# Optimization experiments

Hardware: AMD Instinct MI355X
Metric: run time of the kernel (lower is better)

Reference implementation:

```python
import jax, jax.numpy as jnp
import numpy as np

N_NODES = 100000
N_EDGES = 1600000
D_IN = 128
D_HID = 128
D_OUT = 128
N_LAYERS = 4


def setup_inputs() -> dict:
    key = jax.random.key(0)
    ks = jax.random.split(key, 8)
    x = jax.random.normal(ks[0], (N_NODES, D_IN), dtype=jnp.float32)
    edge_index = jax.random.randint(ks[1], (2, N_EDGES), 0, N_NODES, dtype=jnp.int64)
    s = 1.0 / np.sqrt(D_IN)
    # All layers are 128->128, so stack weights: [L, in, out]
    W_lin = jax.random.uniform(ks[2], (N_LAYERS, D_IN, D_HID), minval=-s, maxval=s, dtype=jnp.float32)
    W_film = jax.random.uniform(ks[3], (N_LAYERS, D_IN, 2 * D_HID), minval=-s, maxval=s, dtype=jnp.float32)
    b_film = jax.random.uniform(ks[4], (N_LAYERS, 2 * D_HID), minval=-s, maxval=s, dtype=jnp.float32)
    W_skip = jax.random.uniform(ks[5], (N_LAYERS, D_IN, D_HID), minval=-s, maxval=s, dtype=jnp.float32)
    W_fskip = jax.random.uniform(ks[6], (N_LAYERS, D_IN, 2 * D_HID), minval=-s, maxval=s, dtype=jnp.float32)
    return {"x": x, "edge_index": edge_index, "W_lin": W_lin, "W_film": W_film,
            "b_film": b_film, "W_skip": W_skip, "W_fskip": W_fskip}


def _film_conv(x, src, dst, deg_inv, W_l, W_f, b_f, W_s, W_fs, c):
    # skip path: FiLM-modulated self transform
    bg_s = x @ W_fs                       # [N, 2C], no bias
    beta_s, gamma_s = bg_s[:, :c], bg_s[:, c:]
    out = jax.nn.relu(gamma_s * (x @ W_s) + beta_s)
    # message path: FiLM params from target node, features from source node
    bg = x @ W_f + b_f                    # [N, 2C]
    beta, gamma = bg[:, :c], bg[:, c:]
    h = x @ W_l                           # [N, C]
    msg = jax.nn.relu(gamma[dst] * h[src] + beta[dst])  # [E, C]
    agg = jax.ops.segment_sum(msg, dst, num_segments=x.shape[0]) * deg_inv  # mean aggr
    return out + agg


def reference(x, edge_index, W_lin, W_film, b_film, W_skip, W_fskip):
    src, dst = edge_index[0], edge_index[1]
    n = x.shape[0]
    deg = jax.ops.segment_sum(jnp.ones((src.shape[0],), x.dtype), dst, num_segments=n)
    deg_inv = (1.0 / jnp.maximum(deg, 1.0))[:, None]   # clamp(min=1) like PyG mean
    for l in range(N_LAYERS):
        x = _film_conv(x, src, dst, deg_inv, W_lin[l], W_film[l], b_film[l],
                       W_skip[l], W_fskip[l], D_HID)
        if l < N_LAYERS - 1:
            x = jax.nn.relu(x)
    return x
```

## Files before the change

### kernel.cpp

```cpp
#include <hip/hip_runtime.h>
#include <hip/hip_bf16.h>

#define N_NODES 100000
#define N_PAD   100096
#define N_EDGES 1600000
#define NXCD    8
#define NRANGE  ((N_NODES + NXCD - 1) / NXCD)
#define NSLICE  256
#define MTILES  (N_PAD / 128)
#define MTQ     ((MTILES + 7) / 8)
#define GEMM_GRID (8 * 7 * MTQ)

typedef __bf16 bf16x8 __attribute__((ext_vector_type(8)));
typedef float  f32x4  __attribute__((ext_vector_type(4)));

__device__ __forceinline__ void gload16(const void* g, void* s) {
    __builtin_amdgcn_global_load_lds(
        (const __attribute__((address_space(1))) unsigned int*)g,
        (__attribute__((address_space(3))) unsigned int*)s, 16, 0, 0);
}

__device__ __forceinline__ float2 bf2f(unsigned p) {
    float2 r;
    union { unsigned u; float f; } a, b;
    a.u = p << 16;
    b.u = p & 0xffff0000u;
    r.x = a.f; r.y = b.f;
    return r;
}
__device__ __forceinline__ unsigned f2bf2(float x, float y) {
    unsigned lo = (unsigned)__builtin_bit_cast(unsigned short, __float2bfloat16(x));
    unsigned hi = (unsigned)__builtin_bit_cast(unsigned short, __float2bfloat16(y));
    return lo | (hi << 16);
}

__global__ void detect_kernel(const unsigned* __restrict__ e, int* __restrict__ flag) {
    __shared__ int nz;
    if (threadIdx.x == 0) nz = 0;
    __syncthreads();
    int local = 0;
    for (int i = threadIdx.x; i < 1024; i += blockDim.x)
        if (e[2 * i + 1] != 0) local = 1;
    if (local) atomicOr(&nz, 1);
    __syncthreads();
    if (threadIdx.x == 0) *flag = (nz == 0) ? 1 : 0;
}

__device__ __forceinline__ int edge_at(const unsigned* __restrict__ e, long idx, int is64) {
    return (int)(is64 ? e[2 * idx] : e[idx]);
}

__global__ void hist_kernel(const unsigned* __restrict__ e, const int* __restrict__ flag,
                            int* __restrict__ counts) {
    int i = blockIdx.x * blockDim.x + threadIdx.x;
    if (i >= N_EDGES) return;
    int is64 = *flag;
    int d = edge_at(e, (long)N_EDGES + i, is64);
    atomicAdd(&counts[d], 1);
}

__global__ void scan1_kernel(const int* __restrict__ counts, int* __restrict__ blockSums) {
    __shared__ int red[256];
    int base = blockIdx.x * 1024;
    int sum = 0;
    for (int i = threadIdx.x; i < 1024; i += 256) {
        int idx = base + i;
        sum += (idx < N_NODES) ? counts[idx] : 0;
    }
    red[threadIdx.x] = sum;
    __syncthreads();
    for (int s = 128; s > 0; s >>= 1) {
        if (threadIdx.x < s) red[threadIdx.x] += red[threadIdx.x + s];
        __syncthreads();
    }
    if (threadIdx.x == 0) blockSums[blockIdx.x] = red[0];
}

__global__ void scan2_kernel(int* __restrict__ blockSums, int nb, int* __restrict__ row_ptr) {
    int run = 0;
    for (int i = 0; i < nb; ++i) { int v = blockSums[i]; blockSums[i] = run; run += v; }
    row_ptr[N_NODES] = run;
}

__global__ void scan3_kernel(const int* __restrict__ counts, const int* __restrict__ blockSums,
                             int* __restrict__ row_ptr, int* __restrict__ cursor,
                             float* __restrict__ deg_inv) {
    __shared__ int lds[256];
    int base = blockIdx.x * 1024;
    int t = threadIdx.x;
    int v[4];
    int s = 0;
    for (int i = 0; i < 4; ++i) {
        int idx = base + t * 4 + i;
        v[i] = (idx < N_NODES) ? counts[idx] : 0;
        s += v[i];
    }
    lds[t] = s;
    __syncthreads();
    for (int off = 1; off < 256; off <<= 1) {
        int add = (t >= off) ? lds[t - off] : 0;
        __syncthreads();
        lds[t] += add;
        __syncthreads();
    }
    int excl = lds[t] - s + blockSums[blockIdx.x];
    for (int i = 0; i < 4; ++i) {
        int idx = base + t * 4 + i;
        if (idx < N_NODES) {
            row_ptr[idx] = excl;
            cursor[idx]  = excl;
            deg_inv[idx] = 1.0f / fmaxf((float)v[i], 1.0f);
            excl += v[i];
        }
    }
}

__global__ __launch_bounds__(256) void fill2_kernel(
    const unsigned* __restrict__ e, const int* __restrict__ flag,
    int* __restrict__ cursor, int* __restrict__ csr_src) {
    const int r     = blockIdx.x & (NXCD - 1);
    const int slice = blockIdx.x >> 3;
    const int lo = r * NRANGE;
    const int hi = min(lo + NRANGE, N_NODES);
    const int is64 = *flag;
    const int per = (N_EDGES + NSLICE - 1) / NSLICE;
    const int i0 = slice * per;
    const int i1 = min(i0 + per, N_EDGES);
    for (int i = i0 + (int)threadIdx.x; i < i1; i += 256) {
        int d = edge_at(e, (long)N_EDGES + i, is64);
        if (d >= lo && d < hi) {
            int s = edge_at(e, (long)i, is64);
            int pos = atomicAdd(&cursor[d], 1);
            csr_src[pos] = s;
        }
    }
}

__global__ void bt_prep_kernel(const float* __restrict__ Wl, const float* __restrict__ Wf,
                               const float* __restrict__ Ws, const float* __restrict__ Wfs,
                               __hip_bfloat16* __restrict__ Bt) {
    int idx = blockIdx.x * 256 + threadIdx.x;
    if (idx >= 4 * 768 * 128) return;
    int k   = idx % 128;
    int row = (idx / 128) % 768;
    int lay = idx / (128 * 768);
    float w;
    if (row < 128) {
        w = Wl[(size_t)lay * 16384 + k * 128 + row];
    } else if (row < 384) {
        w = Wf[(size_t)lay * 32768 + k * 256 + (row - 128)];
    } else {
        int rr = row - 384;
        int g = rr >> 4, within = rr & 15;
        int kind = g % 3;
        int c = (g / 3) * 16 + within;
        if (kind == 0)      w = Ws [(size_t)lay * 16384 + k * 128 + c];
        else if (kind == 1) w = Wfs[(size_t)lay * 32768 + k * 256 + c];
        else                w = Wfs[(size_t)lay * 32768 + k * 256 + 128 + c];
    }
    Bt[idx] = __float2bfloat16(w);
}

__global__ void cast_kernel(const float* __restrict__ x, unsigned* __restrict__ A2) {
    long i = (long)blockIdx.x * 256 + threadIdx.x;
    if (i >= (long)N_NODES * 64) return;
    float2 v = ((const float2*)x)[i];
    A2[i] = f2bf2(v.x, v.y);
}

__global__ __launch_bounds__(256, 2) void fused_gemm_kernel(
    const __hip_bfloat16* __restrict__ A,
    const __hip_bfloat16* __restrict__ Bt,
    const float* __restrict__ bfilm,
    __hip_bfloat16* __restrict__ hbuf,
    __hip_bfloat16* __restrict__ bgbuf,
    __hip_bfloat16* __restrict__ skbh)
{
    __shared__ alignas(16) unsigned char lds_raw[32768];
    unsigned char* ldsA = lds_raw;
    unsigned char* ldsB = lds_raw + 16384;

    const int b   = blockIdx.x;
    const int r8  = b & 7;
    const int q   = b >> 3;
    const int jt  = q % 7;
    const int mt  = (q / 7) * 8 + r8;
    if (mt >= MTILES) return;

    const int t  = threadIdx.x;
    const long node0 = (long)mt * 128;
    const int w  = t >> 6, l = t & 63;
    const int wm = w >> 1, wn = w & 1;
    const int lr = l & 15;
    const int kq16 = (l >> 4) << 4;
    const int sw = (lr & 7) << 4;

    const int sr  = t >> 3;
    const int scb = (t & 7) << 4;
    const int scbs = scb ^ ((sr & 7) << 4);

    const char* Abase = (const char*)A;

    if (jt < 3) {
        const char* Bbase = (const char*)Bt + (size_t)(jt * 128) * 256;
        f32x4 acc[4][4];
        #pragma unroll
        for (int mi = 0; mi < 4; ++mi)
            #pragma unroll
            for (int ni = 0; ni < 4; ++ni)
                #pragma unroll
                for (int j = 0; j < 4; ++j) acc[mi][ni][j] = 0.f;

        #pragma unroll
        for (int ks = 0; ks < 2; ++ks) {
            const int k0 = ks * 64;
            #pragma unroll
            for (int i = 0; i < 4; ++i) {
                const int r = (i << 5) + sr;
                gload16(Abase + (node0 + r) * 256 + (size_t)k0 * 2 + scbs,
                        ldsA + (((i << 8) + t) << 4));
                gload16(Bbase + (size_t)r * 256 + (size_t)k0 * 2 + scbs,
                        ldsB + (((i << 8) + t) << 4));
            }
            __syncthreads();

            #pragma unroll
            for (int kh = 0; kh < 2; ++kh) {
                const int kbs = ((kh << 6) + kq16) ^ sw;
                bf16x8 af[4], bfr[4];
                #pragma unroll
                for (int mi = 0; mi < 4; ++mi)
                    af[mi] = *(const bf16x8*)(ldsA + (wm * 64 + mi * 16 + lr) * 128 + kbs);
                #pragma unroll
                for (int ni = 0; ni < 4; ++ni)
                    bfr[ni] = *(const bf16x8*)(ldsB + (wn * 64 + ni * 16 + lr) * 128 + kbs);
                #pragma unroll
                for (int mi = 0; mi < 4; ++mi)
                    #pragma unroll
                    for (int ni = 0; ni < 4; ++ni)
                        acc[mi][ni] = __builtin_amdgcn_mfma_f32_16x16x32_bf16(
                            af[mi], bfr[ni], acc[mi][ni], 0, 0, 0);
            }
            __syncthreads();
        }

        const int col = lr;
        const int rb  = (l >> 4) << 2;
        if (jt == 0) {
            #pragma unroll
            for (int mi = 0; mi < 4; ++mi)
                #pragma unroll
                for (int ni = 0; ni < 4; ++ni) {
                    const int n = wn * 64 + ni * 16 + col;
                    #pragma unroll
                    for (int j = 0; j < 4; ++j) {
                        long node = node0 + wm * 64 + mi * 16 + rb + j;
                        if (node < N_NODES)
                            hbuf[node * 128 + n] = __float2bfloat16(acc[mi][ni][j]);
                    }
                }
        } else {
            const int c0 = (jt - 1) * 128;
            #pragma unroll
            for (int mi = 0; mi < 4; ++mi)
                #pragma unroll
                for (int ni = 0; ni < 4; ++ni) {
                    const int n = wn * 64 + ni * 16 + col;
                    const float bb = bfilm[c0 + n];
                    #pragma unroll
                    for (int j = 0; j < 4; ++j) {
                        long node = node0 + wm * 64 + mi * 16 + rb + j;
                        if (node < N_NODES)
                            bgbuf[node * 256 + c0 + n] = __float2bfloat16(acc[mi][ni][j] + bb);
                    }
                }
        }
    } else {
        const int jt2 = jt - 3;
        const char* Bbase = (const char*)Bt + (size_t)(384 + jt2 * 96) * 256;
        f32x4 acc[4][3];
        #pragma unroll
        for (int mi = 0; mi < 4; ++mi)
            #pragma unroll
            for (int ni = 0; ni < 3; ++ni)
                #pragma unroll
                for (int j = 0; j < 4; ++j) acc[mi][ni][j] = 0.f;

        #pragma unroll
        for (int ks = 0; ks < 2; ++ks) {
            const int k0 = ks * 64;
            #pragma unroll
            for (int i = 0; i < 4; ++i) {
                const int r = (i << 5) + sr;
                gload16(Abase + (node0 + r) * 256 + (size_t)k0 * 2 + scbs,
                        ldsA + (((i << 8) + t) << 4));
            }
            #pragma unroll
            for (int i = 0; i < 3; ++i) {
                const int r = (i << 5) + sr;
                gload16(Bbase + (size_t)r * 256 + (size_t)k0 * 2 + scbs,
                        ldsB + (((i << 8) + t) << 4));
            }
            __syncthreads();

            #pragma unroll
            for (int kh = 0; kh < 2; ++kh) {
                const int kbs = ((kh << 6) + kq16) ^ sw;
                bf16x8 af[4], bfr[3];
                #pragma unroll
                for (int mi = 0; mi < 4; ++mi)
                    af[mi] = *(const bf16x8*)(ldsA + (wm * 64 + mi * 16 + lr) * 128 + kbs);
                #pragma unroll
                for (int ni = 0; ni < 3; ++ni)
                    bfr[ni] = *(const bf16x8*)(ldsB + (wn * 48 + ni * 16 + lr) * 128 + kbs);
                #pragma unroll
                for (int mi = 0; mi < 4; ++mi)
                    #pragma unroll
                    for (int ni = 0; ni < 3; ++ni)
                        acc[mi][ni] = __builtin_amdgcn_mfma_f32_16x16x32_bf16(
                            af[mi], bfr[ni], acc[mi][ni], 0, 0, 0);
            }
            __syncthreads();
        }

        const int c  = (2 * jt2 + wn) * 16 + lr;
        const int rb = (l >> 4) << 2;
        #pragma unroll
        for (int mi = 0; mi < 4; ++mi)
            #pragma unroll
            for (int j = 0; j < 4; ++j) {
                long node = node0 + wm * 64 + mi * 16 + rb + j;
                if (node < N_NODES) {
                    float o = fmaxf(acc[mi][2][j] * acc[mi][0][j] + acc[mi][1][j], 0.f);
                    skbh[node * 128 + c] = __float2bfloat16(o);
                }
            }
    }
}

__global__ __launch_bounds__(256) void agg_kernel(
    const uint2* __restrict__ h22,
    const uint2* __restrict__ bgu2,
    const int* __restrict__ row_ptr, const int* __restrict__ csr_src,
    const float* __restrict__ deg_inv,
    const uint2* __restrict__ sku2,
    uint2* __restrict__ An2,
    float4* __restrict__ fo4)
{
    const int t = threadIdx.x;
    const int v = blockIdx.x * 4 + (t >> 6);
    const int l = t & 63;
    const int half = l >> 5;
    const unsigned c = l & 31;

    const uint2 bu = bgu2[(size_t)v * 64 + c];
    const uint2 gu = bgu2[(size_t)v * 64 + 32 + c];
    const float2 be01 = bf2f(bu.x), be23 = bf2f(bu.y);
    const float2 ga01 = bf2f(gu.x), ga23 = bf2f(gu.y);
    const float dinv = deg_inv[v];

    const int b = row_ptr[v];
    const int e = row_ptr[v + 1];
    const int ne = e - b;
    const int npair = ne >> 1;

    f32x4 ac0 = {0,0,0,0}, ac1 = {0,0,0,0}, ac2 = {0,0,0,0}, ac3 = {0,0,0,0};

    const int* cp = csr_src + b + half;

#define ACC(A_, P_) do {                                   \
        float2 h01 = bf2f((P_).x), h23 = bf2f((P_).y);     \
        (A_)[0] += fmaxf(ga01.x * h01.x + be01.x, 0.f);    \
        (A_)[1] += fmaxf(ga01.y * h01.y + be01.y, 0.f);    \
        (A_)[2] += fmaxf(ga23.x * h23.x + be23.x, 0.f);    \
        (A_)[3] += fmaxf(ga23.y * h23.y + be23.y, 0.f);    \
    } while (0)

    int pi = 0;
    for (; pi + 8 <= npair; pi += 8) {
        unsigned s[8];
        uint2 p[8];
        #pragma unroll
        for (int u = 0; u < 8; ++u) s[u] = (unsigned)cp[2 * (pi + u)];
        #pragma unroll
        for (int u = 0; u < 8; ++u) p[u] = h22[s[u] * 32u + c];
        ACC(ac0, p[0]); ACC(ac1, p[1]); ACC(ac2, p[2]); ACC(ac3, p[3]);
        ACC(ac0, p[4]); ACC(ac1, p[5]); ACC(ac2, p[6]); ACC(ac3, p[7]);
    }
    for (; pi + 4 <= npair; pi += 4) {
        unsigned s[4];
        uint2 p[4];
        #pragma unroll
        for (int u = 0; u < 4; ++u) s[u] = (unsigned)cp[2 * (pi + u)];
        #pragma unroll
        for (int u = 0; u < 4; ++u) p[u] = h22[s[u] * 32u + c];
        ACC(ac0, p[0]); ACC(ac1, p[1]); ACC(ac2, p[2]); ACC(ac3, p[3]);
    }
    for (; pi < npair; ++pi) {
        const unsigned s0 = (unsigned)cp[2 * pi];
        const uint2 p0 = h22[s0 * 32u + c];
        ACC(ac0, p0);
    }
    if ((ne & 1) && half == 0) {
        const unsigned s0 = (unsigned)csr_src[e - 1];
        const uint2 p0 = h22[s0 * 32u + c];
        ACC(ac1, p0);
    }
#undef ACC

    float r0 = (ac0[0] + ac1[0]) + (ac2[0] + ac3[0]);
    float r1 = (ac0[1] + ac1[1]) + (ac2[1] + ac3[1]);
    float r2 = (ac0[2] + ac1[2]) + (ac2[2] + ac3[2]);
    float r3 = (ac0[3] + ac1[3]) + (ac2[3] + ac3[3]);
    r0 += __shfl_xor(r0, 32);
    r1 += __shfl_xor(r1, 32);
    r2 += __shfl_xor(r2, 32);
    r3 += __shfl_xor(r3, 32);

    const uint2 sk = sku2[(size_t)v * 32 + c];
    const float2 s01 = bf2f(sk.x), s23 = bf2f(sk.y);
    const float o0 = s01.x + r0 * dinv;
    const float o1 = s01.y + r1 * dinv;
    const float o2 = s23.x + r2 * dinv;
    const float o3 = s23.y + r3 * dinv;

    if (half == 0) {
        if (An2) {
            An2[(size_t)v * 32 + c] = make_uint2(f2bf2(o0, o1), f2bf2(o2, o3));
        } else {
            fo4[(size_t)v * 32 + c] = make_float4(o0, o1, o2, o3);
        }
    }
}

extern "C" void kernel_launch(void* const* d_in, const int* in_sizes, int n_in,
                              void* d_out, int out_size, void* d_ws, size_t ws_size,
                              hipStream_t stream) {
    const float*    x_in    = (const float*)d_in[0];
    const unsigned* eidx    = (const unsigned*)d_in[1];
    const float*    W_lin   = (const float*)d_in[2];
    const float*    W_film  = (const float*)d_in[3];
    const float*    b_film  = (const float*)d_in[4];
    const float*    W_skip  = (const float*)d_in[5];
    const float*    W_fskip = (const float*)d_in[6];
    float*          out     = (float*)d_out;

    char* ws = (char*)d_ws;
    size_t off = 0;
    auto alloc = [&](size_t bytes) -> void* {
        void* p = ws + off;
        off = (off + bytes + 255) & ~(size_t)255;
        return p;
    };
    int*   flag      = (int*)alloc(4);
    int*   counts    = (int*)alloc((size_t)N_NODES * 4);
    int*   row_ptr   = (int*)alloc((size_t)(N_NODES + 1) * 4);
    int*   cursor    = (int*)alloc((size_t)N_NODES * 4);
    int*   blockSums = (int*)alloc(128 * 4);
    float* deg_inv   = (float*)alloc((size_t)N_NODES * 4);
    int*   csr_src   = (int*)alloc((size_t)N_EDGES * 4);
    __hip_bfloat16* Abuf  = (__hip_bfloat16*)alloc((size_t)N_PAD * 128 * 2);
    __hip_bfloat16* BtAll = (__hip_bfloat16*)alloc((size_t)4 * 768 * 128 * 2);
    __hip_bfloat16* hbuf  = (__hip_bfloat16*)alloc((size_t)N_NODES * 128 * 2);
    __hip_bfloat16* bgbuf = (__hip_bfloat16*)alloc((size_t)N_NODES * 256 * 2);
    __hip_bfloat16* skbh  = (__hip_bfloat16*)alloc((size_t)N_NODES * 128 * 2);
    (void)ws_size; (void)in_sizes; (void)n_in; (void)out_size;

    const int NB_SCAN = (N_NODES + 1023) / 1024;
    const int EB = (N_EDGES + 255) / 256;

    hipMemsetAsync(counts, 0, (size_t)N_NODES * 4, stream);
    detect_kernel<<<1, 256, 0, stream>>>(eidx, flag);
    hist_kernel<<<EB, 256, 0, stream>>>(eidx, flag, counts);
    scan1_kernel<<<NB_SCAN, 256, 0, stream>>>(counts, blockSums);
    scan2_kernel<<<1, 1, 0, stream>>>(blockSums, NB_SCAN, row_ptr);
    scan3_kernel<<<NB_SCAN, 256, 0, stream>>>(counts, blockSums, row_ptr, cursor, deg_inv);
    fill2_kernel<<<NXCD * NSLICE, 256, 0, stream>>>(eidx, flag, cursor, csr_src);

    cast_kernel<<<(N_NODES * 64 + 255) / 256, 256, 0, stream>>>(x_in, (unsigned*)Abuf);
    bt_prep_kernel<<<(4 * 768 * 128 + 255) / 256, 256, 0, stream>>>(
        W_lin, W_film, W_skip, W_fskip, BtAll);

    const int AGG_B = N_NODES / 4;
    for (int l = 0; l < 4; ++l) {
        const __hip_bfloat16* Bt_l = BtAll + (size_t)l * 768 * 128;
        fused_gemm_kernel<<<GEMM_GRID, 256, 0, stream>>>(
            Abuf, Bt_l, b_film + (size_t)l * 256, hbuf, bgbuf, skbh);
        agg_kernel<<<AGG_B, 256, 0, stream>>>(
            (const uint2*)hbuf, (const uint2*)bgbuf,
            row_ptr, csr_src, deg_inv, (const uint2*)skbh,
            (l < 3) ? (uint2*)Abuf : (uint2*)nullptr,
            (l == 3) ? (float4*)out : (float4*)nullptr);
    }
}
```

Measured before the change: 615.7 us.

## Widen aggregation gathers to 16B, fold deg_inv into FiLM params, XCD-partitioned histogram

The aggregation kernel now handles four edges at once per wavefront. Each 16-lane group gathers a full 256-byte h row with uint4 loads, and the CSR stores precomputed byte offsets (src<<8) so no multiply is needed. The per-node mean scaling is folded into beta/gamma in the GEMM epilogue. This is valid because relu(a)*d = relu(a*d) for d>0, so agg no longer multiplies by deg_inv. The histogram is partitioned by destination range per XCD slice, as fill already was, to keep atomics local. Risks: the offset encoding overflows for large node counts, and reduction across quads adds extra shuffles.

```diff
diff --git a/kernel.cpp b/kernel.cpp
--- a/kernel.cpp
+++ b/kernel.cpp
@@ -50,13 +50,21 @@
     return (int)(is64 ? e[2 * idx] : e[idx]);
 }
 
-__global__ void hist_kernel(const unsigned* __restrict__ e, const int* __restrict__ flag,
-                            int* __restrict__ counts) {
-    int i = blockIdx.x * blockDim.x + threadIdx.x;
-    if (i >= N_EDGES) return;
-    int is64 = *flag;
-    int d = edge_at(e, (long)N_EDGES + i, is64);
-    atomicAdd(&counts[d], 1);
+__global__ __launch_bounds__(256) void hist2_kernel(
+    const unsigned* __restrict__ e, const int* __restrict__ flag,
+    int* __restrict__ counts) {
+    const int r     = blockIdx.x & (NXCD - 1);
+    const int slice = blockIdx.x >> 3;
+    const int lo = r * NRANGE;
+    const int hi = min(lo + NRANGE, N_NODES);
+    const int is64 = *flag;
+    const int per = (N_EDGES + NSLICE - 1) / NSLICE;
+    const int i0 = slice * per;
+    const int i1 = min(i0 + per, N_EDGES);
+    for (int i = i0 + (int)threadIdx.x; i < i1; i += 256) {
+        int d = edge_at(e, (long)N_EDGES + i, is64);
+        if (d >= lo && d < hi) atomicAdd(&counts[d], 1);
+    }
 }
 
 __global__ void scan1_kernel(const int* __restrict__ counts, int* __restrict__ blockSums) {
@@ -117,7 +125,7 @@
 
 __global__ __launch_bounds__(256) void fill2_kernel(
     const unsigned* __restrict__ e, const int* __restrict__ flag,
-    int* __restrict__ cursor, int* __restrict__ csr_src) {
+    int* __restrict__ cursor, int* __restrict__ csr_off) {
     const int r     = blockIdx.x & (NXCD - 1);
     const int slice = blockIdx.x >> 3;
     const int lo = r * NRANGE;
@@ -131,7 +139,7 @@
         if (d >= lo && d < hi) {
             int s = edge_at(e, (long)i, is64);
             int pos = atomicAdd(&cursor[d], 1);
-            csr_src[pos] = s;
+            csr_off[pos] = s << 8;
         }
     }
 }
@@ -172,6 +180,7 @@
     const __hip_bfloat16* __restrict__ A,
     const __hip_bfloat16* __restrict__ Bt,
     const float* __restrict__ bfilm,
+    const float* __restrict__ deg_inv,
     __hip_bfloat16* __restrict__ hbuf,
     __hip_bfloat16* __restrict__ bgbuf,
     __hip_bfloat16* __restrict__ skbh)
@@ -264,14 +273,16 @@
             #pragma unroll
             for (int mi = 0; mi < 4; ++mi)
                 #pragma unroll
-                for (int ni = 0; ni < 4; ++ni) {
-                    const int n = wn * 64 + ni * 16 + col;
-                    const float bb = bfilm[c0 + n];
-                    #pragma unroll
-                    for (int j = 0; j < 4; ++j) {
-                        long node = node0 + wm * 64 + mi * 16 + rb + j;
-                        if (node < N_NODES)
-                            bgbuf[node * 256 + c0 + n] = __float2bfloat16(acc[mi][ni][j] + bb);
+                for (int j = 0; j < 4; ++j) {
+                    long node = node0 + wm * 64 + mi * 16 + rb + j;
+                    if (node < N_NODES) {
+                        const float dv = deg_inv[node];
+                        #pragma unroll
+                        for (int ni = 0; ni < 4; ++ni) {
+                            const int n = wn * 64 + ni * 16 + col;
+                            bgbuf[node * 256 + c0 + n] =
+                                __float2bfloat16((acc[mi][ni][j] + bfilm[c0 + n]) * dv);
+                        }
                     }
                 }
         }
@@ -339,96 +350,104 @@
 }
 
 __global__ __launch_bounds__(256) void agg_kernel(
-    const uint2* __restrict__ h22,
-    const uint2* __restrict__ bgu2,
-    const int* __restrict__ row_ptr, const int* __restrict__ csr_src,
-    const float* __restrict__ deg_inv,
-    const uint2* __restrict__ sku2,
-    uint2* __restrict__ An2,
+    const char* __restrict__ hb,
+    const uint4* __restrict__ bgq,
+    const int* __restrict__ row_ptr, const int* __restrict__ csr_off,
+    const uint4* __restrict__ skq,
+    uint4* __restrict__ An4,
     float4* __restrict__ fo4)
 {
     const int t = threadIdx.x;
     const int v = blockIdx.x * 4 + (t >> 6);
     const int l = t & 63;
-    const int half = l >> 5;
-    const unsigned c = l & 31;
-
-    const uint2 bu = bgu2[(size_t)v * 64 + c];
-    const uint2 gu = bgu2[(size_t)v * 64 + 32 + c];
-    const float2 be01 = bf2f(bu.x), be23 = bf2f(bu.y);
-    const float2 ga01 = bf2f(gu.x), ga23 = bf2f(gu.y);
-    const float dinv = deg_inv[v];
+    const int q = l >> 4;
+    const int cq = l & 15;
+    const int coff = cq << 4;
+
+    const uint4 bu = bgq[(size_t)v * 32 + cq];
+    const uint4 gu = bgq[(size_t)v * 32 + 16 + cq];
+    float be[8], ga[8];
+    {
+        float2 f;
+        f = bf2f(bu.x); be[0] = f.x; be[1] = f.y;
+        f = bf2f(bu.y); be[2] = f.x; be[3] = f.y;
+        f = bf2f(bu.z); be[4] = f.x; be[5] = f.y;
+        f = bf2f(bu.w); be[6] = f.x; be[7] = f.y;
+        f = bf2f(gu.x); ga[0] = f.x; ga[1] = f.y;
+        f = bf2f(gu.y); ga[2] = f.x; ga[3] = f.y;
+        f = bf2f(gu.z); ga[4] = f.x; ga[5] = f.y;
+        f = bf2f(gu.w); ga[6] = f.x; ga[7] = f.y;
+    }
 
     const int b = row_ptr[v];
     const int e = row_ptr[v + 1];
     const int ne = e - b;
-    const int npair = ne >> 1;
-
-    f32x4 ac0 = {0,0,0,0}, ac1 = {0,0,0,0}, ac2 = {0,0,0,0}, ac3 = {0,0,0,0};
-
-    const int* cp = csr_src + b + half;
-
-#define ACC(A_, P_) do {                                   \
-        float2 h01 = bf2f((P_).x), h23 = bf2f((P_).y);     \
-        (A_)[0] += fmaxf(ga01.x * h01.x + be01.x, 0.f);    \
-        (A_)[1] += fmaxf(ga01.y * h01.y + be01.y, 0.f);    \
-        (A_)[2] += fmaxf(ga23.x * h23.x + be23.x, 0.f);    \
-        (A_)[3] += fmaxf(ga23.y * h23.y + be23.y, 0.f);    \
+    const int ng = ne >> 2;
+    const int tail = ne & 3;
+    const int* cp = csr_off + b;
+
+    float a[8] = {0.f, 0.f, 0.f, 0.f, 0.f, 0.f, 0.f, 0.f};
+
+#define ACC(P_) do {                                               \
+        float2 h01 = bf2f((P_).x), h23 = bf2f((P_).y);             \
+        float2 h45 = bf2f((P_).z), h67 = bf2f((P_).w);             \
+        a[0] += fmaxf(ga[0] * h01.x + be[0], 0.f);                 \
+        a[1] += fmaxf(ga[1] * h01.y + be[1], 0.f);                 \
+        a[2] += fmaxf(ga[2] * h23.x + be[2], 0.f);                 \
+        a[3] += fmaxf(ga[3] * h23.y + be[3], 0.f);                 \
+        a[4] += fmaxf(ga[4] * h45.x + be[4], 0.f);                 \
+        a[5] += fmaxf(ga[5] * h45.y + be[5], 0.f);                 \
+        a[6] += fmaxf(ga[6] * h67.x + be[6], 0.f);                 \
+        a[7] += fmaxf(ga[7] * h67.y + be[7], 0.f);                 \
     } while (0)
 
-    int pi = 0;
-    for (; pi + 8 <= npair; pi += 8) {
-        unsigned s[8];
-        uint2 p[8];
-        #pragma unroll
-        for (int u = 0; u < 8; ++u) s[u] = (unsigned)cp[2 * (pi + u)];
-        #pragma unroll
-        for (int u = 0; u < 8; ++u) p[u] = h22[s[u] * 32u + c];
-        ACC(ac0, p[0]); ACC(ac1, p[1]); ACC(ac2, p[2]); ACC(ac3, p[3]);
-        ACC(ac0, p[4]); ACC(ac1, p[5]); ACC(ac2, p[6]); ACC(ac3, p[7]);
-    }
-    for (; pi + 4 <= npair; pi += 4) {
-        unsigned s[4];
-        uint2 p[4];
-        #pragma unroll
-        for (int u = 0; u < 4; ++u) s[u] = (unsigned)cp[2 * (pi + u)];
-        #pragma unroll
-        for (int u = 0; u < 4; ++u) p[u] = h22[s[u] * 32u + c];
-        ACC(ac0, p[0]); ACC(ac1, p[1]); ACC(ac2, p[2]); ACC(ac3, p[3]);
-    }
-    for (; pi < npair; ++pi) {
-        const unsigned s0 = (unsigned)cp[2 * pi];
-        const uint2 p0 = h22[s0 * 32u + c];
-        ACC(ac0, p0);
-    }
-    if ((ne & 1) && half == 0) {
-        const unsigned s0 = (unsigned)csr_src[e - 1];
-        const uint2 p0 = h22[s0 * 32u + c];
-        ACC(ac1, p0);
+    int g = 0;
+    for (; g + 4 <= ng; g += 4) {
+        const unsigned o0 = (unsigned)cp[(g    ) * 4 + q] + coff;
+        const unsigned o1 = (unsigned)cp[(g + 1) * 4 + q] + coff;
+        const unsigned o2 = (unsigned)cp[(g + 2) * 4 + q] + coff;
+        const unsigned o3 = (unsigned)cp[(g + 3) * 4 + q] + coff;
+        const uint4 p0 = *(const uint4*)(hb + o0);
+        const uint4 p1 = *(const uint4*)(hb + o1);
+        const uint4 p2 = *(const uint4*)(hb + o2);
+        const uint4 p3 = *(const uint4*)(hb + o3);
+        ACC(p0); ACC(p1); ACC(p2); ACC(p3);
+    }
+    for (; g < ng; ++g) {
+        const unsigned o0 = (unsigned)cp[g * 4 + q] + coff;
+        const uint4 p0 = *(const uint4*)(hb + o0);
+        ACC(p0);
+    }
+    if (tail) {
+        const bool valid = q < tail;
+        const unsigned o0 = (unsigned)cp[valid ? (ng * 4 + q) : 0] + coff;
+        const uint4 p0 = *(const uint4*)(hb + o0);
+        if (valid) ACC(p0);
     }
 #undef ACC
 
-    float r0 = (ac0[0] + ac1[0]) + (ac2[0] + ac3[0]);
-    float r1 = (ac0[1] + ac1[1]) + (ac2[1] + ac3[1]);
-    float r2 = (ac0[2] + ac1[2]) + (ac2[2] + ac3[2]);
-    float r3 = (ac0[3] + ac1[3]) + (ac2[3] + ac3[3]);
-    r0 += __shfl_xor(r0, 32);
-    r1 += __shfl_xor(r1, 32);
-    r2 += __shfl_xor(r2, 32);
-    r3 += __shfl_xor(r3, 32);
-
-    const uint2 sk = sku2[(size_t)v * 32 + c];
-    const float2 s01 = bf2f(sk.x), s23 = bf2f(sk.y);
-    const float o0 = s01.x + r0 * dinv;
-    const float o1 = s01.y + r1 * dinv;
-    const float o2 = s23.x + r2 * dinv;
-    const float o3 = s23.y + r3 * dinv;
-
-    if (half == 0) {
-        if (An2) {
-            An2[(size_t)v * 32 + c] = make_uint2(f2bf2(o0, o1), f2bf2(o2, o3));
+    #pragma unroll
+    for (int i = 0; i < 8; ++i) {
+        a[i] += __shfl_xor(a[i], 16);
+        a[i] += __shfl_xor(a[i], 32);
+    }
+
+    if (q == 0) {
+        const uint4 sk = skq[(size_t)v * 16 + cq];
+        const float2 s01 = bf2f(sk.x), s23 = bf2f(sk.y);
+        const float2 s45 = bf2f(sk.z), s67 = bf2f(sk.w);
+        const float o0 = s01.x + a[0], o1 = s01.y + a[1];
+        const float o2 = s23.x + a[2], o3 = s23.y + a[3];
+        const float o4 = s45.x + a[4], o5 = s45.y + a[5];
+        const float o6 = s67.x + a[6], o7 = s67.y + a[7];
+        if (An4) {
+            uint4 r;
+            r.x = f2bf2(o0, o1); r.y = f2bf2(o2, o3);
+            r.z = f2bf2(o4, o5); r.w = f2bf2(o6, o7);
+            An4[(size_t)v * 16 + cq] = r;
         } else {
-            fo4[(size_t)v * 32 + c] = make_float4(o0, o1, o2, o3);
+            fo4[(size_t)v * 32 + 2 * cq]     = make_float4(o0, o1, o2, o3);
+            fo4[(size_t)v * 32 + 2 * cq + 1] = make_float4(o4, o5, o6, o7);
         }
     }
 }
@@ -458,7 +477,7 @@
     int*   cursor    = (int*)alloc((size_t)N_NODES * 4);
     int*   blockSums = (int*)alloc(128 * 4);
     float* deg_inv   = (float*)alloc((size_t)N_NODES * 4);
-    int*   csr_src   = (int*)alloc((size_t)N_EDGES * 4);
+    int*   csr_off   = (int*)alloc((size_t)N_EDGES * 4);
     __hip_bfloat16* Abuf  = (__hip_bfloat16*)alloc((size_t)N_PAD * 128 * 2);
     __hip_bfloat16* BtAll = (__hip_bfloat16*)alloc((size_t)4 * 768 * 128 * 2);
     __hip_bfloat16* hbuf  = (__hip_bfloat16*)alloc((size_t)N_NODES * 128 * 2);
@@ -467,15 +486,14 @@
     (void)ws_size; (void)in_sizes; (void)n_in; (void)out_size;
 
     const int NB_SCAN = (N_NODES + 1023) / 1024;
-    const int EB = (N_EDGES + 255) / 256;
 
     hipMemsetAsync(counts, 0, (size_t)N_NODES * 4, stream);
     detect_kernel<<<1, 256, 0, stream>>>(eidx, flag);
-    hist_kernel<<<EB, 256, 0, stream>>>(eidx, flag, counts);
+    hist2_kernel<<<NXCD * NSLICE, 256, 0, stream>>>(eidx, flag, counts);
     scan1_kernel<<<NB_SCAN, 256, 0, stream>>>(counts, blockSums);
     scan2_kernel<<<1, 1, 0, stream>>>(blockSums, NB_SCAN, row_ptr);
     scan3_kernel<<<NB_SCAN, 256, 0, stream>>>(counts, blockSums, row_ptr, cursor, deg_inv);
-    fill2_kernel<<<NXCD * NSLICE, 256, 0, stream>>>(eidx, flag, cursor, csr_src);
+    fill2_kernel<<<NXCD * NSLICE, 256, 0, stream>>>(eidx, flag, cursor, csr_off);
 
     cast_kernel<<<(N_NODES * 64 + 255) / 256, 256, 0, stream>>>(x_in, (unsigned*)Abuf);
     bt_prep_kernel<<<(4 * 768 * 128 + 255) / 256, 256, 0, stream>>>(
@@ -485,11 +503,11 @@
     for (int l = 0; l < 4; ++l) {
         const __hip_bfloat16* Bt_l = BtAll + (size_t)l * 768 * 128;
         fused_gemm_kernel<<<GEMM_GRID, 256, 0, stream>>>(
-            Abuf, Bt_l, b_film + (size_t)l * 256, hbuf, bgbuf, skbh);
+            Abuf, Bt_l, b_film + (size_t)l * 256, deg_inv, hbuf, bgbuf, skbh);
         agg_kernel<<<AGG_B, 256, 0, stream>>>(
-            (const uint2*)hbuf, (const uint2*)bgbuf,
-            row_ptr, csr_src, deg_inv, (const uint2*)skbh,
-            (l < 3) ? (uint2*)Abuf : (uint2*)nullptr,
+            (const char*)hbuf, (const uint4*)bgbuf,
+            row_ptr, csr_off, (const uint4*)skbh,
+            (l < 3) ? (uint4*)Abuf : (uint4*)nullptr,
             (l == 3) ? (float4*)out : (float4*)nullptr);
     }
 }
```

Result: slower. 667.5 us (+8.4%).

## Fold degree normalization into FiLM params, prescale CSR offsets, XCD-partition histogram

Applied to the files above, without the earlier changes.

The mean normalization is folded into beta and gamma in the GEMM epilogue. Since relu(g*h+b)*d equals relu(d*g*h+d*b) for positive d, the aggregation kernel no longer loads or applies deg_inv. CSR entries now store byte offsets (src<<8) so the gather skips an index multiply. The degree histogram uses the same XCD-range partitioning as the fill kernel to keep its atomics local. The cost is that bf16 rounding of the scaled FiLM parameters changes slightly, and the epilogue's store loop order changes, which may affect store coalescing.

```diff
diff --git a/kernel.cpp b/kernel.cpp
--- a/kernel.cpp
+++ b/kernel.cpp
@@ -50,13 +50,21 @@
     return (int)(is64 ? e[2 * idx] : e[idx]);
 }
 
-__global__ void hist_kernel(const unsigned* __restrict__ e, const int* __restrict__ flag,
-                            int* __restrict__ counts) {
-    int i = blockIdx.x * blockDim.x + threadIdx.x;
-    if (i >= N_EDGES) return;
-    int is64 = *flag;
-    int d = edge_at(e, (long)N_EDGES + i, is64);
-    atomicAdd(&counts[d], 1);
+__global__ __launch_bounds__(256) void hist2_kernel(
+    const unsigned* __restrict__ e, const int* __restrict__ flag,
+    int* __restrict__ counts) {
+    const int r     = blockIdx.x & (NXCD - 1);
+    const int slice = blockIdx.x >> 3;
+    const int lo = r * NRANGE;
+    const int hi = min(lo + NRANGE, N_NODES);
+    const int is64 = *flag;
+    const int per = (N_EDGES + NSLICE - 1) / NSLICE;
+    const int i0 = slice * per;
+    const int i1 = min(i0 + per, N_EDGES);
+    for (int i = i0 + (int)threadIdx.x; i < i1; i += 256) {
+        int d = edge_at(e, (long)N_EDGES + i, is64);
+        if (d >= lo && d < hi) atomicAdd(&counts[d], 1);
+    }
 }
 
 __global__ void scan1_kernel(const int* __restrict__ counts, int* __restrict__ blockSums) {
@@ -117,7 +125,7 @@
 
 __global__ __launch_bounds__(256) void fill2_kernel(
     const unsigned* __restrict__ e, const int* __restrict__ flag,
-    int* __restrict__ cursor, int* __restrict__ csr_src) {
+    int* __restrict__ cursor, int* __restrict__ csr_off) {
     const int r     = blockIdx.x & (NXCD - 1);
     const int slice = blockIdx.x >> 3;
     const int lo = r * NRANGE;
@@ -131,7 +139,7 @@
         if (d >= lo && d < hi) {
             int s = edge_at(e, (long)i, is64);
             int pos = atomicAdd(&cursor[d], 1);
-            csr_src[pos] = s;
+            csr_off[pos] = s << 8;
         }
     }
 }
@@ -172,6 +180,7 @@
     const __hip_bfloat16* __restrict__ A,
     const __hip_bfloat16* __restrict__ Bt,
     const float* __restrict__ bfilm,
+    const float* __restrict__ deg_inv,
     __hip_bfloat16* __restrict__ hbuf,
     __hip_bfloat16* __restrict__ bgbuf,
     __hip_bfloat16* __restrict__ skbh)
@@ -264,14 +273,16 @@
             #pragma unroll
             for (int mi = 0; mi < 4; ++mi)
                 #pragma unroll
-                for (int ni = 0; ni < 4; ++ni) {
-                    const int n = wn * 64 + ni * 16 + col;
-                    const float bb = bfilm[c0 + n];
-                    #pragma unroll
-                    for (int j = 0; j < 4; ++j) {
-                        long node = node0 + wm * 64 + mi * 16 + rb + j;
-                        if (node < N_NODES)
-                            bgbuf[node * 256 + c0 + n] = __float2bfloat16(acc[mi][ni][j] + bb);
+                for (int j = 0; j < 4; ++j) {
+                    long node = node0 + wm * 64 + mi * 16 + rb + j;
+                    if (node < N_NODES) {
+                        const float dv = deg_inv[node];
+                        #pragma unroll
+                        for (int ni = 0; ni < 4; ++ni) {
+                            const int n = wn * 64 + ni * 16 + col;
+                            bgbuf[node * 256 + c0 + n] =
+                                __float2bfloat16((acc[mi][ni][j] + bfilm[c0 + n]) * dv);
+                        }
                     }
                 }
         }
@@ -339,10 +350,9 @@
 }
 
 __global__ __launch_bounds__(256) void agg_kernel(
-    const uint2* __restrict__ h22,
+    const char* __restrict__ hb,
     const uint2* __restrict__ bgu2,
-    const int* __restrict__ row_ptr, const int* __restrict__ csr_src,
-    const float* __restrict__ deg_inv,
+    const int* __restrict__ row_ptr, const int* __restrict__ csr_off,
     const uint2* __restrict__ sku2,
     uint2* __restrict__ An2,
     float4* __restrict__ fo4)
@@ -352,12 +362,12 @@
     const int l = t & 63;
     const int half = l >> 5;
     const unsigned c = l & 31;
+    const unsigned coff = c << 3;
 
     const uint2 bu = bgu2[(size_t)v * 64 + c];
     const uint2 gu = bgu2[(size_t)v * 64 + 32 + c];
     const float2 be01 = bf2f(bu.x), be23 = bf2f(bu.y);
     const float2 ga01 = bf2f(gu.x), ga23 = bf2f(gu.y);
-    const float dinv = deg_inv[v];
 
     const int b = row_ptr[v];
     const int e = row_ptr[v + 1];
@@ -366,7 +376,7 @@
 
     f32x4 ac0 = {0,0,0,0}, ac1 = {0,0,0,0}, ac2 = {0,0,0,0}, ac3 = {0,0,0,0};
 
-    const int* cp = csr_src + b + half;
+    const int* cp = csr_off + b + half;
 
 #define ACC(A_, P_) do {                                   \
         float2 h01 = bf2f((P_).x), h23 = bf2f((P_).y);     \
@@ -378,32 +388,32 @@
 
     int pi = 0;
     for (; pi + 8 <= npair; pi += 8) {
-        unsigned s[8];
+        unsigned o[8];
         uint2 p[8];
         #pragma unroll
-        for (int u = 0; u < 8; ++u) s[u] = (unsigned)cp[2 * (pi + u)];
-        #pragma unroll
-        for (int u = 0; u < 8; ++u) p[u] = h22[s[u] * 32u + c];
+        for (int u = 0; u < 8; ++u) o[u] = (unsigned)cp[2 * (pi + u)] + coff;
+        #pragma unroll
+        for (int u = 0; u < 8; ++u) p[u] = *(const uint2*)(hb + o[u]);
         ACC(ac0, p[0]); ACC(ac1, p[1]); ACC(ac2, p[2]); ACC(ac3, p[3]);
         ACC(ac0, p[4]); ACC(ac1, p[5]); ACC(ac2, p[6]); ACC(ac3, p[7]);
     }
     for (; pi + 4 <= npair; pi += 4) {
-        unsigned s[4];
+        unsigned o[4];
         uint2 p[4];
         #pragma unroll
-        for (int u = 0; u < 4; ++u) s[u] = (unsigned)cp[2 * (pi + u)];
-        #pragma unroll
-        for (int u = 0; u < 4; ++u) p[u] = h22[s[u] * 32u + c];
+        for (int u = 0; u < 4; ++u) o[u] = (unsigned)cp[2 * (pi + u)] + coff;
+        #pragma unroll
+        for (int u = 0; u < 4; ++u) p[u] = *(const uint2*)(hb + o[u]);
         ACC(ac0, p[0]); ACC(ac1, p[1]); ACC(ac2, p[2]); ACC(ac3, p[3]);
     }
     for (; pi < npair; ++pi) {
-        const unsigned s0 = (unsigned)cp[2 * pi];
-        const uint2 p0 = h22[s0 * 32u + c];
+        const unsigned o0 = (unsigned)cp[2 * pi] + coff;
+        const uint2 p0 = *(const uint2*)(hb + o0);
         ACC(ac0, p0);
     }
     if ((ne & 1) && half == 0) {
-        const unsigned s0 = (unsigned)csr_src[e - 1];
-        const uint2 p0 = h22[s0 * 32u + c];
+        const unsigned o0 = (unsigned)csr_off[e - 1] + coff;
+        const uint2 p0 = *(const uint2*)(hb + o0);
         ACC(ac1, p0);
     }
 #undef ACC
@@ -419,10 +429,10 @@
 
     const uint2 sk = sku2[(size_t)v * 32 + c];
     const float2 s01 = bf2f(sk.x), s23 = bf2f(sk.y);
-    const float o0 = s01.x + r0 * dinv;
-    const float o1 = s01.y + r1 * dinv;
-    const float o2 = s23.x + r2 * dinv;
-    const float o3 = s23.y + r3 * dinv;
+    const float o0 = s01.x + r0;
+    const float o1 = s01.y + r1;
+    const float o2 = s23.x + r2;
+    const float o3 = s23.y + r3;
 
     if (half == 0) {
         if (An2) {
@@ -458,7 +468,7 @@
     int*   cursor    = (int*)alloc((size_t)N_NODES * 4);
     int*   blockSums = (int*)alloc(128 * 4);
     float* deg_inv   = (float*)alloc((size_t)N_NODES * 4);
-    int*   csr_src   = (int*)alloc((size_t)N_EDGES * 4);
+    int*   csr_off   = (int*)alloc((size_t)N_EDGES * 4);
     __hip_bfloat16* Abuf  = (__hip_bfloat16*)alloc((size_t)N_PAD * 128 * 2);
     __hip_bfloat16* BtAll = (__hip_bfloat16*)alloc((size_t)4 * 768 * 128 * 2);
     __hip_bfloat16* hbuf  = (__hip_bfloat16*)alloc((size_t)N_NODES * 128 * 2);
@@ -467,15 +477,14 @@
     (void)ws_size; (void)in_sizes; (void)n_in; (void)out_size;
 
     const int NB_SCAN = (N_NODES + 1023) / 1024;
-    const int EB = (N_EDGES + 255) / 256;
 
     hipMemsetAsync(counts, 0, (size_t)N_NODES * 4, stream);
     detect_kernel<<<1, 256, 0, stream>>>(eidx, flag);
-    hist_kernel<<<EB, 256, 0, stream>>>(eidx, flag, counts);
+    hist2_kernel<<<NXCD * NSLICE, 256, 0, stream>>>(eidx, flag, counts);
     scan1_kernel<<<NB_SCAN, 256, 0, stream>>>(counts, blockSums);
     scan2_kernel<<<1, 1, 0, stream>>>(blockSums, NB_SCAN, row_ptr);
     scan3_kernel<<<NB_SCAN, 256, 0, stream>>>(counts, blockSums, row_ptr, cursor, deg_inv);
-    fill2_kernel<<<NXCD * NSLICE, 256, 0, stream>>>(eidx, flag, cursor, csr_src);
+    fill2_kernel<<<NXCD * NSLICE, 256, 0, stream>>>(eidx, flag, cursor, csr_off);
 
     cast_kernel<<<(N_NODES * 64 + 255) / 256, 256, 0, stream>>>(x_in, (unsigned*)Abuf);
     bt_prep_kernel<<<(4 * 768 * 128 + 255) / 256, 256, 0, stream>>>(
@@ -485,10 +494,10 @@
     for (int l = 0; l < 4; ++l) {
         const __hip_bfloat16* Bt_l = BtAll + (size_t)l * 768 * 128;
         fused_gemm_kernel<<<GEMM_GRID, 256, 0, stream>>>(
-            Abuf, Bt_l, b_film + (size_t)l * 256, hbuf, bgbuf, skbh);
+            Abuf, Bt_l, b_film + (size_t)l * 256, deg_inv, hbuf, bgbuf, skbh);
         agg_kernel<<<AGG_B, 256, 0, stream>>>(
-            (const uint2*)hbuf, (const uint2*)bgbuf,
-            row_ptr, csr_src, deg_inv, (const uint2*)skbh,
+            (const char*)hbuf, (const uint2*)bgbuf,
+            row_ptr, csr_off, (const uint2*)skbh,
             (l < 3) ? (uint2*)Abuf : (uint2*)nullptr,
             (l == 3) ? (float4*)out : (float4*)nullptr);
     }
```

Result: slower. 650.9 us (+5.7%).
